# Kernel tuning notes

Hardware: AMD Instinct MI355X
Metric: run time of the kernel (lower is better)

The kernel has to match this reference:

```python
import jax, jax.numpy as jnp
import numpy as np

IN_C, OUT_C, N = 512, 256, 8192
NEG_INF = -1000000000.0  # matches torch's -1e9 fill


def setup_inputs() -> dict:
    key = jax.random.key(0)
    ks = jax.random.split(key, 8)
    x = jax.random.normal(ks[0], (N, IN_C), dtype=jnp.float32)
    adj = jax.random.randint(ks[1], (N, N), 0, 2, dtype=jnp.int32)
    # fc: Linear(in_c, out_c)
    lim_fc = 1.0 / np.sqrt(IN_C)
    W_fc = jax.random.uniform(ks[2], (IN_C, OUT_C), minval=-lim_fc, maxval=lim_fc, dtype=jnp.float32)
    b_fc = jax.random.uniform(ks[3], (OUT_C,), minval=-lim_fc, maxval=lim_fc, dtype=jnp.float32)
    # a1, a2: Linear(out_c, 1)
    lim_a = 1.0 / np.sqrt(OUT_C)
    W_a1 = jax.random.uniform(ks[4], (OUT_C, 1), minval=-lim_a, maxval=lim_a, dtype=jnp.float32)
    b_a1 = jax.random.uniform(ks[5], (1,), minval=-lim_a, maxval=lim_a, dtype=jnp.float32)
    W_a2 = jax.random.uniform(ks[6], (OUT_C, 1), minval=-lim_a, maxval=lim_a, dtype=jnp.float32)
    b_a2 = jax.random.uniform(ks[7], (1,), minval=-lim_a, maxval=lim_a, dtype=jnp.float32)
    return {"x": x, "adj": adj, "W_fc": W_fc, "b_fc": b_fc,
            "W_a1": W_a1, "b_a1": b_a1, "W_a2": W_a2, "b_a2": b_a2}


def reference(x, adj, W_fc, b_fc, W_a1, b_a1, W_a2, b_a2):
    h = x @ W_fc + b_fc                      # [N, out_c]
    s1 = h @ W_a1 + b_a1                     # [N, 1]
    s2 = h @ W_a2 + b_a2                     # [N, 1]
    e = jax.nn.leaky_relu(s1 + s2.T)         # [N, N], slope 0.01 matches torch default
    att = jnp.where(adj > 0, e, NEG_INF)
    att = jax.nn.softmax(att, axis=1)        # dropout omitted (eval mode)
    return att @ h                           # [N, out_c]
```

## Files before the change

### kernel.cpp

```cpp
#include <hip/hip_runtime.h>
#include <hip/hip_bf16.h>

#define IN_C 512
#define OUT_C 256
#define NN 8192
#define JSPL 4
#define JRANGE (NN / JSPL)
#define NT (JRANGE / 32)
#define L2E 1.44269504088896f

typedef __attribute__((ext_vector_type(8))) short s16x8;
typedef __attribute__((ext_vector_type(4))) float f32x4;

__device__ __forceinline__ ushort f2bf(float f) {
    unsigned u = __float_as_uint(f);
    unsigned r = (u + 0x7FFF + ((u >> 16) & 1)) >> 16;
    return (ushort)r;
}

__global__ __launch_bounds__(256) void fc_kernel(
    const float* __restrict__ x, const float* __restrict__ Wfc,
    const float* __restrict__ bfc, const float* __restrict__ Wa1,
    const float* __restrict__ ba1, const float* __restrict__ Wa2,
    const float* __restrict__ ba2,
    uint4* __restrict__ hb,
    float* __restrict__ s1, float* __restrict__ s2)
{
    __shared__ float xl[8 * IN_C];
    __shared__ float red[2][8][4];
    const int t = threadIdx.x;
    const int r0 = blockIdx.x * 8;

    {
        const float4* src = (const float4*)(x + (size_t)r0 * IN_C);
        float4* dst = (float4*)xl;
        #pragma unroll
        for (int i = 0; i < 4; i++) dst[i * 256 + t] = src[i * 256 + t];
    }
    __syncthreads();

    float acc[8];
    #pragma unroll
    for (int r = 0; r < 8; r++) acc[r] = 0.f;

    for (int c4 = 0; c4 < IN_C / 4; c4++) {
        const float w0 = Wfc[(c4 * 4 + 0) * OUT_C + t];
        const float w1 = Wfc[(c4 * 4 + 1) * OUT_C + t];
        const float w2 = Wfc[(c4 * 4 + 2) * OUT_C + t];
        const float w3 = Wfc[(c4 * 4 + 3) * OUT_C + t];
        #pragma unroll
        for (int r = 0; r < 8; r++) {
            const float4 xv = *(const float4*)&xl[r * IN_C + c4 * 4];
            acc[r] = fmaf(xv.x, w0, acc[r]);
            acc[r] = fmaf(xv.y, w1, acc[r]);
            acc[r] = fmaf(xv.z, w2, acc[r]);
            acc[r] = fmaf(xv.w, w3, acc[r]);
        }
    }
    const float bb = bfc[t];
    #pragma unroll
    for (int r = 0; r < 8; r++) acc[r] += bb;

    {
        union { ushort u[8]; uint4 v; } pk;
        #pragma unroll
        for (int r = 0; r < 8; r++) pk.u[r] = f2bf(acc[r]);
        const int jt = r0 >> 5, u = (r0 >> 3) & 3;
        hb[(size_t)jt * 1024 + u * 256 + t] = pk.v;
    }

    float p1[8], p2[8];
    const float wa1 = Wa1[t], wa2 = Wa2[t];
    #pragma unroll
    for (int r = 0; r < 8; r++) { p1[r] = acc[r] * wa1; p2[r] = acc[r] * wa2; }
    #pragma unroll
    for (int off = 32; off > 0; off >>= 1) {
        #pragma unroll
        for (int r = 0; r < 8; r++) {
            p1[r] += __shfl_down(p1[r], off);
            p2[r] += __shfl_down(p2[r], off);
        }
    }
    const int wv = t >> 6, ln = t & 63;
    if (ln == 0) {
        #pragma unroll
        for (int r = 0; r < 8; r++) { red[0][r][wv] = p1[r]; red[1][r][wv] = p2[r]; }
    }
    __syncthreads();
    if (t < 16) {
        const int s = t >> 3, r = t & 7;
        float v = red[s][r][0] + red[s][r][1] + red[s][r][2] + red[s][r][3];
        v += s ? ba2[0] : ba1[0];
        if (s) s2[r0 + r] = v; else s1[r0 + r] = v;
    }
}

__global__ __launch_bounds__(256) void smax_kernel(const float* __restrict__ s2,
                                                   float* __restrict__ smax)
{
    __shared__ float red[4];
    float m = -1e30f;
    for (int i = threadIdx.x; i < NN; i += 256) m = fmaxf(m, s2[i]);
    #pragma unroll
    for (int off = 32; off > 0; off >>= 1) m = fmaxf(m, __shfl_down(m, off));
    if ((threadIdx.x & 63) == 0) red[threadIdx.x >> 6] = m;
    __syncthreads();
    if (threadIdx.x == 0)
        smax[0] = fmaxf(fmaxf(red[0], red[1]), fmaxf(red[2], red[3]));
}

__global__ __launch_bounds__(512, 4) void attn_kernel(
    const int* __restrict__ adj, const uint4* __restrict__ hb,
    const float* __restrict__ s1, const float* __restrict__ s2,
    const float* __restrict__ smaxp, float* __restrict__ outp,
    float* __restrict__ pbase, float* __restrict__ rs)
{
    __shared__ float s2l[JRANGE];
    __shared__ unsigned long long mask_lds[64][33];

    const int t = threadIdx.x;
    const int wave = t >> 6, lane = t & 63;
    const int wr = wave >> 1;
    const int ch = wave & 1;
    const int g = lane >> 4, lr = lane & 15;
    const int jq = blockIdx.y;
    const int Jbase = jq * JRANGE;
    const int R0 = blockIdx.x * 64;
    const int row = R0 + wr * 16 + lr;

    {
        const float4 v = ((const float4*)(s2 + Jbase))[t];
        ((float4*)s2l)[t] = make_float4(v.x * L2E, v.y * L2E, v.z * L2E, v.w * L2E);
    }

    {
        const int prow0 = wave * 8;
        for (int r = 0; r < 8; ++r) {
            const int* arow = adj + (size_t)(R0 + prow0 + r) * NN + Jbase + lane;
            int v[32];
            #pragma unroll
            for (int c = 0; c < 32; ++c)
                v[c] = __builtin_nontemporal_load(arow + c * 64);
            unsigned long long myw = 0;
            #pragma unroll
            for (int c = 0; c < 32; ++c) {
                const unsigned long long m = __ballot(v[c] > 0);
                if (lane == c) myw = m;
            }
            if (lane < 32) mask_lds[prow0 + r][lane] = myw;
        }
    }

    const float my_s1 = s1[row] * L2E;
    const float z0 = my_s1 + smaxp[0] * L2E;
    const float m_i = fmaxf(z0, 0.01f * z0);

    f32x4 acc[8];
    #pragma unroll
    for (int n = 0; n < 8; n++) acc[n] = (f32x4)(0.f);
    float rsum = 0.f;

    const uint4* hb_base = hb + (size_t)(Jbase >> 5) * 1024 + ch * 128;

    __syncthreads();

    for (int tt = 0; tt < NT; ++tt) {
        const unsigned long long m64 = mask_lds[wr * 16 + lr][tt >> 1];
        const unsigned mb = (unsigned)(m64 >> ((tt & 1) * 32 + g * 8)) & 0xFFu;

        const int j0 = tt * 32 + g * 8;
        const float4 sva = *(const float4*)(s2l + j0);
        const float4 svb = *(const float4*)(s2l + j0 + 4);
        const float sv[8] = {sva.x, sva.y, sva.z, sva.w, svb.x, svb.y, svb.z, svb.w};
        union { ushort u[8]; s16x8 v; } pk;
        #pragma unroll
        for (int e = 0; e < 8; e++) {
            const float zz = my_s1 + sv[e];
            const float ee = fmaxf(zz, 0.01f * zz);
            float p = exp2f(ee - m_i);
            p = ((mb >> e) & 1u) ? p : 0.f;
            rsum += p;
            pk.u[e] = f2bf(p);
        }
        const s16x8 afrag = pk.v;

        const uint4* bsrc = hb_base + (size_t)tt * 1024 + g * 256 + lr;
        uint4 bf[4];
        #pragma unroll
        for (int n = 0; n < 4; n++) bf[n] = bsrc[n * 16];
        #pragma unroll
        for (int n = 0; n < 4; n++)
            acc[n] = __builtin_amdgcn_mfma_f32_16x16x32_bf16(afrag, *(const s16x8*)&bf[n], acc[n], 0, 0, 0);
        #pragma unroll
        for (int n = 0; n < 4; n++) bf[n] = bsrc[64 + n * 16];
        #pragma unroll
        for (int n = 0; n < 4; n++)
            acc[n + 4] = __builtin_amdgcn_mfma_f32_16x16x32_bf16(afrag, *(const s16x8*)&bf[n], acc[n + 4], 0, 0, 0);
    }

    rsum += __shfl_xor(rsum, 16);
    rsum += __shfl_xor(rsum, 32);
    if (ch == 0 && g == 0) rs[(size_t)jq * NN + row] = rsum;

    float* dst = (jq == 0) ? outp : (pbase + (size_t)(jq - 1) * ((size_t)NN * OUT_C));
    #pragma unroll
    for (int r = 0; r < 4; r++) {
        const int orow = R0 + wr * 16 + g * 4 + r;
        float* op = dst + (size_t)orow * OUT_C + ch * 128 + lr;
        #pragma unroll
        for (int n = 0; n < 8; n++)
            __builtin_nontemporal_store(acc[n][r], op + n * 16);
    }
}

__global__ __launch_bounds__(256) void combine_kernel(
    float* __restrict__ out, const float* __restrict__ pbase,
    const float* __restrict__ rs)
{
    const int row = blockIdx.x, t = threadIdx.x;
    float rsum = 0.f;
    #pragma unroll
    for (int q = 0; q < JSPL; q++) rsum += rs[(size_t)q * NN + row];
    const float inv = 1.f / rsum;
    const size_t idx = (size_t)row * OUT_C + t;
    const size_t stride = (size_t)NN * OUT_C;
    float v = out[idx];
    #pragma unroll
    for (int q = 0; q < JSPL - 1; q++)
        v += __builtin_nontemporal_load(&pbase[idx + (size_t)q * stride]);
    out[idx] = v * inv;
}

extern "C" void kernel_launch(void* const* d_in, const int* in_sizes, int n_in,
                              void* d_out, int out_size, void* d_ws, size_t ws_size,
                              hipStream_t stream) {
    const float* x   = (const float*)d_in[0];
    const int*   adj = (const int*)d_in[1];
    const float* Wfc = (const float*)d_in[2];
    const float* bfc = (const float*)d_in[3];
    const float* Wa1 = (const float*)d_in[4];
    const float* ba1 = (const float*)d_in[5];
    const float* Wa2 = (const float*)d_in[6];
    const float* ba2 = (const float*)d_in[7];
    float* out = (float*)d_out;

    char* ws = (char*)d_ws;
    uint4* hb   = (uint4*)ws;
    float* s1   = (float*)(ws + (4u << 20));
    float* s2   = s1 + NN;
    float* rs   = s2 + NN;
    float* smax = rs + JSPL * NN;
    float* pbase = (float*)(ws + (5u << 20));

    fc_kernel<<<dim3(NN / 8), 256, 0, stream>>>(x, Wfc, bfc, Wa1, ba1, Wa2, ba2, hb, s1, s2);
    smax_kernel<<<dim3(1), 256, 0, stream>>>(s2, smax);
    attn_kernel<<<dim3(NN / 64, JSPL), 512, 0, stream>>>(adj, hb, s1, s2, smax, out, pbase, rs);
    combine_kernel<<<dim3(NN), 256, 0, stream>>>(out, pbase, rs);
}
```

Measured before the change: 191.6 us.

## Split attention into separate P-matrix build and bf16 GEMM kernels

```diff
diff --git a/kernel.cpp b/kernel.cpp
--- a/kernel.cpp
+++ b/kernel.cpp
@@ -4,13 +4,14 @@
 #define IN_C 512
 #define OUT_C 256
 #define NN 8192
-#define JSPL 4
-#define JRANGE (NN / JSPL)
-#define NT (JRANGE / 32)
+#define KSPL 4
+#define KRANGE (NN / KSPL)
 #define L2E 1.44269504088896f
 
 typedef __attribute__((ext_vector_type(8))) short s16x8;
 typedef __attribute__((ext_vector_type(4))) float f32x4;
+typedef __attribute__((ext_vector_type(4))) int i32x4;
+typedef __attribute__((ext_vector_type(2))) unsigned int u32x2;
 
 __device__ __forceinline__ ushort f2bf(float f) {
     unsigned u = __float_as_uint(f);
@@ -109,100 +110,121 @@
         smax[0] = fmaxf(fmaxf(red[0], red[1]), fmaxf(red[2], red[3]));
 }
 
-__global__ __launch_bounds__(512, 4) void attn_kernel(
-    const int* __restrict__ adj, const uint4* __restrict__ hb,
-    const float* __restrict__ s1, const float* __restrict__ s2,
-    const float* __restrict__ smaxp, float* __restrict__ outp,
-    float* __restrict__ pbase, float* __restrict__ rs)
-{
-    __shared__ float s2l[JRANGE];
-    __shared__ unsigned long long mask_lds[64][33];
-
-    const int t = threadIdx.x;
-    const int wave = t >> 6, lane = t & 63;
-    const int wr = wave >> 1;
-    const int ch = wave & 1;
-    const int g = lane >> 4, lr = lane & 15;
-    const int jq = blockIdx.y;
-    const int Jbase = jq * JRANGE;
-    const int R0 = blockIdx.x * 64;
-    const int row = R0 + wr * 16 + lr;
-
-    {
-        const float4 v = ((const float4*)(s2 + Jbase))[t];
-        ((float4*)s2l)[t] = make_float4(v.x * L2E, v.y * L2E, v.z * L2E, v.w * L2E);
-    }
-
-    {
-        const int prow0 = wave * 8;
-        for (int r = 0; r < 8; ++r) {
-            const int* arow = adj + (size_t)(R0 + prow0 + r) * NN + Jbase + lane;
-            int v[32];
-            #pragma unroll
-            for (int c = 0; c < 32; ++c)
-                v[c] = __builtin_nontemporal_load(arow + c * 64);
-            unsigned long long myw = 0;
-            #pragma unroll
-            for (int c = 0; c < 32; ++c) {
-                const unsigned long long m = __ballot(v[c] > 0);
-                if (lane == c) myw = m;
-            }
-            if (lane < 32) mask_lds[prow0 + r][lane] = myw;
-        }
-    }
+__global__ __launch_bounds__(256, 8) void pbuild_kernel(
+    const int* __restrict__ adj, const float* __restrict__ s1,
+    const float* __restrict__ s2, const float* __restrict__ smaxp,
+    ushort* __restrict__ P, float* __restrict__ rs)
+{
+    const int wave = threadIdx.x >> 6, lane = threadIdx.x & 63;
+    const int row = blockIdx.x * 4 + wave;
 
     const float my_s1 = s1[row] * L2E;
     const float z0 = my_s1 + smaxp[0] * L2E;
     const float m_i = fmaxf(z0, 0.01f * z0);
 
+    const i32x4*  arow = (const i32x4*)(adj + (size_t)row * NN) + lane;
+    const float4* srow = (const float4*)s2 + lane;
+    ushort* prow = P + (size_t)row * NN;
+    float rsum = 0.f;
+
+#define PPROC(AV, SV, C)                                                        \
+    {                                                                           \
+        const int ai[4] = {AV.x, AV.y, AV.z, AV.w};                             \
+        const float si[4] = {SV.x, SV.y, SV.z, SV.w};                           \
+        ushort pb[4];                                                           \
+        _Pragma("unroll")                                                       \
+        for (int e = 0; e < 4; e++) {                                           \
+            const float zz = fmaf(si[e], L2E, my_s1);                           \
+            const float ee = fmaxf(zz, 0.01f * zz);                             \
+            float p = exp2f(ee - m_i);                                          \
+            p = (ai[e] > 0) ? p : 0.f;                                          \
+            rsum += p;                                                          \
+            pb[e] = f2bf(p);                                                    \
+        }                                                                       \
+        u32x2 w;                                                                \
+        w.x = (unsigned)pb[0] | ((unsigned)pb[1] << 16);                        \
+        w.y = (unsigned)pb[2] | ((unsigned)pb[3] << 16);                        \
+        __builtin_nontemporal_store(w, (u32x2*)(prow + (C) * 256 + lane * 4));  \
+    }
+
+    i32x4 Aa = __builtin_nontemporal_load(arow);
+    float4 Sa = srow[0];
+    i32x4 Ab = __builtin_nontemporal_load(arow + 64);
+    float4 Sb = srow[64];
+    #pragma unroll 1
+    for (int i = 0; i < 16; ++i) {
+        const int c0 = 2 * i, c1 = 2 * i + 1;
+        PPROC(Aa, Sa, c0)
+        {
+            const int cn = (c0 + 2 < 32) ? c0 + 2 : 0;
+            Aa = __builtin_nontemporal_load(arow + cn * 64);
+            Sa = srow[cn * 64];
+        }
+        PPROC(Ab, Sb, c1)
+        {
+            const int cn = (c1 + 2 < 32) ? c1 + 2 : 0;
+            Ab = __builtin_nontemporal_load(arow + cn * 64);
+            Sb = srow[cn * 64];
+        }
+    }
+#undef PPROC
+
+    #pragma unroll
+    for (int off = 32; off > 0; off >>= 1) rsum += __shfl_down(rsum, off);
+    if (lane == 0) rs[row] = rsum;
+}
+
+__global__ __launch_bounds__(256, 4) void pgemm_kernel(
+    const ushort* __restrict__ P, const uint4* __restrict__ hb,
+    float* __restrict__ outp, float* __restrict__ pbase)
+{
+    const int t = threadIdx.x;
+    const int wave = t >> 6, lane = t & 63;
+    const int wr = wave >> 1, ch = wave & 1;
+    const int g = lane >> 4, lr = lane & 15;
+    const int kq = blockIdx.y;
+    const int kbase = kq * KRANGE;
+    const int R0 = blockIdx.x * 32;
+    const int row = R0 + wr * 16 + lr;
+
+    const i32x4* arow = (const i32x4*)(P + (size_t)row * NN + kbase + g * 8);
+    const uint4* hbb = hb + (size_t)(kbase >> 5) * 1024 + g * 256 + ch * 128 + lr;
+
     f32x4 acc[8];
     #pragma unroll
     for (int n = 0; n < 8; n++) acc[n] = (f32x4)(0.f);
-    float rsum = 0.f;
-
-    const uint4* hb_base = hb + (size_t)(Jbase >> 5) * 1024 + ch * 128;
-
-    __syncthreads();
-
-    for (int tt = 0; tt < NT; ++tt) {
-        const unsigned long long m64 = mask_lds[wr * 16 + lr][tt >> 1];
-        const unsigned mb = (unsigned)(m64 >> ((tt & 1) * 32 + g * 8)) & 0xFFu;
-
-        const int j0 = tt * 32 + g * 8;
-        const float4 sva = *(const float4*)(s2l + j0);
-        const float4 svb = *(const float4*)(s2l + j0 + 4);
-        const float sv[8] = {sva.x, sva.y, sva.z, sva.w, svb.x, svb.y, svb.z, svb.w};
-        union { ushort u[8]; s16x8 v; } pk;
-        #pragma unroll
-        for (int e = 0; e < 8; e++) {
-            const float zz = my_s1 + sv[e];
-            const float ee = fmaxf(zz, 0.01f * zz);
-            float p = exp2f(ee - m_i);
-            p = ((mb >> e) & 1u) ? p : 0.f;
-            rsum += p;
-            pk.u[e] = f2bf(p);
-        }
-        const s16x8 afrag = pk.v;
-
-        const uint4* bsrc = hb_base + (size_t)tt * 1024 + g * 256 + lr;
-        uint4 bf[4];
-        #pragma unroll
-        for (int n = 0; n < 4; n++) bf[n] = bsrc[n * 16];
-        #pragma unroll
-        for (int n = 0; n < 4; n++)
-            acc[n] = __builtin_amdgcn_mfma_f32_16x16x32_bf16(afrag, *(const s16x8*)&bf[n], acc[n], 0, 0, 0);
-        #pragma unroll
-        for (int n = 0; n < 4; n++) bf[n] = bsrc[64 + n * 16];
-        #pragma unroll
-        for (int n = 0; n < 4; n++)
-            acc[n + 4] = __builtin_amdgcn_mfma_f32_16x16x32_bf16(afrag, *(const s16x8*)&bf[n], acc[n + 4], 0, 0, 0);
-    }
-
-    rsum += __shfl_xor(rsum, 16);
-    rsum += __shfl_xor(rsum, 32);
-    if (ch == 0 && g == 0) rs[(size_t)jq * NN + row] = rsum;
-
-    float* dst = (jq == 0) ? outp : (pbase + (size_t)(jq - 1) * ((size_t)NN * OUT_C));
+
+    i32x4 A0 = __builtin_nontemporal_load(arow + 0);
+    i32x4 A1 = __builtin_nontemporal_load(arow + 4);
+    i32x4 A2 = __builtin_nontemporal_load(arow + 8);
+    i32x4 A3 = __builtin_nontemporal_load(arow + 12);
+
+#define GBODY(K, KT)                                                            \
+    {                                                                           \
+        const s16x8 afrag = *(const s16x8*)&A##K;                               \
+        const uint4* bsrc = hbb + (size_t)(KT) * 1024;                          \
+        uint4 bf[8];                                                            \
+        _Pragma("unroll")                                                       \
+        for (int n = 0; n < 8; n++) bf[n] = bsrc[n * 16];                       \
+        _Pragma("unroll")                                                       \
+        for (int n = 0; n < 8; n++)                                             \
+            acc[n] = __builtin_amdgcn_mfma_f32_16x16x32_bf16(                   \
+                afrag, *(const s16x8*)&bf[n], acc[n], 0, 0, 0);                 \
+        const int tn = ((KT) + 4 < KRANGE / 32) ? (KT) + 4 : 0;                 \
+        A##K = __builtin_nontemporal_load(arow + tn * 4);                       \
+    }
+
+    #pragma unroll 1
+    for (int i = 0; i < KRANGE / 32 / 4; ++i) {
+        const int tb = i * 4;
+        GBODY(0, tb + 0)
+        GBODY(1, tb + 1)
+        GBODY(2, tb + 2)
+        GBODY(3, tb + 3)
+    }
+#undef GBODY
+
+    float* dst = (kq == 0) ? outp : (pbase + (size_t)(kq - 1) * ((size_t)NN * OUT_C));
     #pragma unroll
     for (int r = 0; r < 4; r++) {
         const int orow = R0 + wr * 16 + g * 4 + r;
@@ -218,15 +240,12 @@
     const float* __restrict__ rs)
 {
     const int row = blockIdx.x, t = threadIdx.x;
-    float rsum = 0.f;
-    #pragma unroll
-    for (int q = 0; q < JSPL; q++) rsum += rs[(size_t)q * NN + row];
-    const float inv = 1.f / rsum;
+    const float inv = 1.f / rs[row];
     const size_t idx = (size_t)row * OUT_C + t;
     const size_t stride = (size_t)NN * OUT_C;
     float v = out[idx];
     #pragma unroll
-    for (int q = 0; q < JSPL - 1; q++)
+    for (int q = 0; q < KSPL - 1; q++)
         v += __builtin_nontemporal_load(&pbase[idx + (size_t)q * stride]);
     out[idx] = v * inv;
 }
@@ -249,11 +268,13 @@
     float* s1   = (float*)(ws + (4u << 20));
     float* s2   = s1 + NN;
     float* rs   = s2 + NN;
-    float* smax = rs + JSPL * NN;
+    float* smax = rs + NN;
     float* pbase = (float*)(ws + (5u << 20));
+    ushort* P   = (ushort*)(ws + (32u << 20));
 
     fc_kernel<<<dim3(NN / 8), 256, 0, stream>>>(x, Wfc, bfc, Wa1, ba1, Wa2, ba2, hb, s1, s2);
     smax_kernel<<<dim3(1), 256, 0, stream>>>(s2, smax);
-    attn_kernel<<<dim3(NN / 64, JSPL), 512, 0, stream>>>(adj, hb, s1, s2, smax, out, pbase, rs);
+    pbuild_kernel<<<dim3(NN / 4), 256, 0, stream>>>(adj, s1, s2, smax, P, rs);
+    pgemm_kernel<<<dim3(NN / 32, KSPL), 256, 0, stream>>>(P, hb, out, pbase);
     combine_kernel<<<dim3(NN), 256, 0, stream>>>(out, pbase, rs);
 }
```

Result: slower. 313.7 us (+63.7%).
